# Optimization experiments

Hardware: AMD Instinct MI355X
Metric: run time of the kernel (lower is better)

The kernel has to match this reference:

```python
import jax, jax.numpy as jnp
import numpy as np


def setup_inputs() -> dict:
    key = jax.random.key(0)
    k1, k2, k3 = jax.random.split(key, 3)
    B, M, J = 4096, 64, 24  # batch, n_max_markers, n_joints
    points = jax.random.normal(k1, (B, M, 3), dtype=jnp.float32)
    weight = jax.random.uniform(k2, (B, M, J), dtype=jnp.float32)  # positive soft weights
    offset = jax.random.normal(k3, (B, M, J, 3), dtype=jnp.float32)
    return {"points": points, "weight": weight, "offset": offset}


def reference(points, weight, offset):
    # P: per-joint marker offsets (B, J, 3, M); Q: world marker positions (B, 1, 3, M)
    P = jnp.transpose(offset, (0, 2, 3, 1))
    Q = jnp.transpose(points, (0, 2, 1))[:, None]
    w = jnp.transpose(weight, (0, 2, 1))[:, :, None]  # (B, J, 1, M)

    wsum = jnp.sum(w, axis=-1)                   # (B, J, 1)
    P_ = jnp.sum(P * w, axis=-1) / wsum          # (B, J, 3) weighted centroid of offsets
    Q_ = jnp.sum(Q * w, axis=-1) / wsum          # (B, J, 3) weighted centroid of markers

    X = P - P_[..., None]                        # (B, J, 3, M)
    Y = Q - Q_[..., None]                        # (B, J, 3, M) via broadcast

    # Cross-covariance S = X @ Y^T (NOTE: original multiplies un-weighted centered coords)
    S = jnp.einsum('bjdm,bjem->bjde', X, Y)      # (B, J, 3, 3)

    U, _, Vh = jnp.linalg.svd(S)
    V = jnp.swapaxes(Vh, -1, -2)
    Ut = jnp.swapaxes(U, -1, -2)
    det = jnp.linalg.det(jnp.matmul(V, Ut))      # (B, J) reflection correction
    Ut = Ut.at[..., -1, :].multiply(det[..., None])
    R = jnp.matmul(V, Ut)                        # (B, J, 3, 3) optimal rotation
    t = Q_[..., None] - jnp.matmul(R, P_[..., None])  # (B, J, 3, 1)
    return R, t
```

## Files before the change

### kernel.cpp

```cpp
#include <hip/hip_runtime.h>


constexpr int M = 64;
constexpr int J = 24;
constexpr int NACC = 22;
constexpr int NWS  = 15;

constexpr int L4_W = 0;
constexpr int L4_O = 384;
constexpr int L4_P = 1536;
constexpr int L4_N = 1584;

__global__ __launch_bounds__(256, 4) void accum_kernel(
    const float* __restrict__ points,
    const float* __restrict__ weight,
    const float* __restrict__ offset,
    float* __restrict__ ws,
    int bj_total)
{
    const int b = blockIdx.x;
    const int t = threadIdx.x;

    __shared__ float4 lds4[L4_N];

    const float4* wb4 = (const float4*)(weight + (size_t)b * (M * J));
    const float4* ob4 = (const float4*)(offset + (size_t)b * (M * J * 3));
    const float4* pb4 = (const float4*)(points + (size_t)b * (M * 3));

    float4 o0_ = ob4[t];
    float4 o1_ = ob4[t + 256];
    float4 o2_ = ob4[t + 512];
    float4 o3_ = ob4[t + 768];
    float4 w0_ = wb4[t];
    float4 o4_ = {0.f, 0.f, 0.f, 0.f};
    float4 w1_ = {0.f, 0.f, 0.f, 0.f};
    float4 p0_ = {0.f, 0.f, 0.f, 0.f};
    if (t < 128) { o4_ = ob4[1024 + t]; w1_ = wb4[256 + t]; }
    if (t < 48)  { p0_ = pb4[t]; }

    lds4[L4_O + t]        = o0_;
    lds4[L4_O + 256 + t]  = o1_;
    lds4[L4_O + 512 + t]  = o2_;
    lds4[L4_O + 768 + t]  = o3_;
    lds4[L4_W + t]        = w0_;
    if (t < 128) { lds4[L4_O + 1024 + t] = o4_; lds4[L4_W + 256 + t] = w1_; }
    if (t < 48)  { lds4[L4_P + t] = p0_; }

    __syncthreads();

    const int lane = t & 63;
    const int wv   = t >> 6;
    const int kk   = lane & 7;
    const int jj   = (lane >> 3) + wv * 8;
    if (jj >= J) return;

    const float* w_s = (const float*)lds4;
    const float* o_s = (const float*)lds4 + 4 * L4_O;
    const float* p_s = (const float*)lds4 + 4 * L4_P;

    float acc[NACC];
#pragma unroll
    for (int n = 0; n < NACC; ++n) acc[n] = 0.0f;

#pragma unroll
    for (int i = 0; i < M / 8; ++i) {
        const int m = i * 8 + kk;
        float w  = w_s[m * J + jj];
        float o0 = o_s[m * 72 + jj * 3 + 0];
        float o1 = o_s[m * 72 + jj * 3 + 1];
        float o2 = o_s[m * 72 + jj * 3 + 2];
        float p0 = p_s[m * 3 + 0];
        float p1 = p_s[m * 3 + 1];
        float p2 = p_s[m * 3 + 2];
        acc[0] += w;
        acc[1] = fmaf(w, o0, acc[1]);  acc[2] = fmaf(w, o1, acc[2]);  acc[3] = fmaf(w, o2, acc[3]);
        acc[4] = fmaf(w, p0, acc[4]);  acc[5] = fmaf(w, p1, acc[5]);  acc[6] = fmaf(w, p2, acc[6]);
        acc[7] += o0; acc[8] += o1; acc[9] += o2;
        acc[10] += p0; acc[11] += p1; acc[12] += p2;
        acc[13] = fmaf(o0, p0, acc[13]); acc[14] = fmaf(o0, p1, acc[14]); acc[15] = fmaf(o0, p2, acc[15]);
        acc[16] = fmaf(o1, p0, acc[16]); acc[17] = fmaf(o1, p1, acc[17]); acc[18] = fmaf(o1, p2, acc[18]);
        acc[19] = fmaf(o2, p0, acc[19]); acc[20] = fmaf(o2, p1, acc[20]); acc[21] = fmaf(o2, p2, acc[21]);
    }

#pragma unroll
    for (int n = 0; n < NACC; ++n) {
        float v = acc[n];
        v += __shfl_xor(v, 1);
        v += __shfl_xor(v, 2);
        v += __shfl_xor(v, 4);
        acc[n] = v;
    }

    if (kk != 0) return;

    const float inv = __builtin_amdgcn_rcpf(acc[0]);
    const float cP0 = acc[1] * inv, cP1 = acc[2] * inv, cP2 = acc[3] * inv;
    const float cQ0 = acc[4] * inv, cQ1 = acc[5] * inv, cQ2 = acc[6] * inv;
    const float To0 = acc[7], To1 = acc[8], To2 = acc[9];
    const float Tp0 = acc[10], Tp1 = acc[11], Tp2 = acc[12];
    const float fM = (float)M;
    float Sv[NWS];
    Sv[0] = acc[13] - cP0 * Tp0 - cQ0 * To0 + fM * cP0 * cQ0;
    Sv[1] = acc[14] - cP0 * Tp1 - cQ1 * To0 + fM * cP0 * cQ1;
    Sv[2] = acc[15] - cP0 * Tp2 - cQ2 * To0 + fM * cP0 * cQ2;
    Sv[3] = acc[16] - cP1 * Tp0 - cQ0 * To1 + fM * cP1 * cQ0;
    Sv[4] = acc[17] - cP1 * Tp1 - cQ1 * To1 + fM * cP1 * cQ1;
    Sv[5] = acc[18] - cP1 * Tp2 - cQ2 * To1 + fM * cP1 * cQ2;
    Sv[6] = acc[19] - cP2 * Tp0 - cQ0 * To2 + fM * cP2 * cQ0;
    Sv[7] = acc[20] - cP2 * Tp1 - cQ1 * To2 + fM * cP2 * cQ1;
    Sv[8] = acc[21] - cP2 * Tp2 - cQ2 * To2 + fM * cP2 * cQ2;
    Sv[9]  = cP0; Sv[10] = cP1; Sv[11] = cP2;
    Sv[12] = cQ0; Sv[13] = cQ1; Sv[14] = cQ2;

    const int bj = b * J + jj;
#pragma unroll
    for (int n = 0; n < NWS; ++n) ws[(size_t)n * bj_total + bj] = Sv[n];
}

template<int P, int Q>
__device__ __forceinline__ void jrot(float A[4][4], float V[4][4]) {
    float apq = A[P][Q];
    float theta = (A[Q][Q] - A[P][P]) * __builtin_amdgcn_rcpf(2.0f * apq);
    float t = __builtin_amdgcn_rcpf(fabsf(theta) + __builtin_amdgcn_sqrtf(fmaf(theta, theta, 1.0f)));
    t = (theta < 0.0f) ? -t : t;
    t = (apq == 0.0f) ? 0.0f : t;
    float c = __builtin_amdgcn_rsqf(fmaf(t, t, 1.0f));
    float s = t * c;
#pragma unroll
    for (int k = 0; k < 4; ++k) {
        float akp = A[k][P], akq = A[k][Q];
        A[k][P] = c * akp - s * akq;
        A[k][Q] = s * akp + c * akq;
    }
#pragma unroll
    for (int k = 0; k < 4; ++k) {
        float apk = A[P][k], aqk = A[Q][k];
        A[P][k] = c * apk - s * aqk;
        A[Q][k] = s * apk + c * aqk;
        float vkp = V[k][P], vkq = V[k][Q];
        V[k][P] = c * vkp - s * vkq;
        V[k][Q] = s * vkp + c * vkq;
    }
}

__device__ __forceinline__ void horn_solve(
    float S00, float S01, float S02, float S10, float S11, float S12,
    float S20, float S21, float S22,
    float cP0, float cP1, float cP2, float cQ0, float cQ1, float cQ2,
    float* __restrict__ Rout, float* __restrict__ tout)
{
    float A[4][4], V[4][4];
    A[0][0] = S00 + S11 + S22;
    A[0][1] = A[1][0] = S12 - S21;
    A[0][2] = A[2][0] = S20 - S02;
    A[0][3] = A[3][0] = S01 - S10;
    A[1][1] = S00 - S11 - S22;
    A[1][2] = A[2][1] = S01 + S10;
    A[1][3] = A[3][1] = S02 + S20;
    A[2][2] = -S00 + S11 - S22;
    A[2][3] = A[3][2] = S12 + S21;
    A[3][3] = -S00 - S11 + S22;
#pragma unroll
    for (int r = 0; r < 4; ++r)
#pragma unroll
        for (int c = 0; c < 4; ++c)
            V[r][c] = (r == c) ? 1.0f : 0.0f;

#pragma unroll 1
    for (int sweep = 0; sweep < 6; ++sweep) {
        jrot<0, 1>(A, V); jrot<0, 2>(A, V); jrot<0, 3>(A, V);
        jrot<1, 2>(A, V); jrot<1, 3>(A, V); jrot<2, 3>(A, V);
    }

    float best = A[0][0];
    float qw = V[0][0], qx = V[1][0], qy = V[2][0], qz = V[3][0];
#pragma unroll
    for (int i = 1; i < 4; ++i) {
        bool better = A[i][i] > best;
        best = better ? A[i][i] : best;
        qw = better ? V[0][i] : qw;
        qx = better ? V[1][i] : qx;
        qy = better ? V[2][i] : qy;
        qz = better ? V[3][i] : qz;
    }
    float nrm = __builtin_amdgcn_rsqf(qw * qw + qx * qx + qy * qy + qz * qz);
    qw *= nrm; qx *= nrm; qy *= nrm; qz *= nrm;

    float R00 = 1.f - 2.f * (qy * qy + qz * qz);
    float R01 = 2.f * (qx * qy - qw * qz);
    float R02 = 2.f * (qx * qz + qw * qy);
    float R10 = 2.f * (qx * qy + qw * qz);
    float R11 = 1.f - 2.f * (qx * qx + qz * qz);
    float R12 = 2.f * (qy * qz - qw * qx);
    float R20 = 2.f * (qx * qz - qw * qy);
    float R21 = 2.f * (qy * qz + qw * qx);
    float R22 = 1.f - 2.f * (qx * qx + qy * qy);

    Rout[0] = R00; Rout[1] = R01; Rout[2] = R02;
    Rout[3] = R10; Rout[4] = R11; Rout[5] = R12;
    Rout[6] = R20; Rout[7] = R21; Rout[8] = R22;
    tout[0] = cQ0 - (R00 * cP0 + R01 * cP1 + R02 * cP2);
    tout[1] = cQ1 - (R10 * cP0 + R11 * cP1 + R12 * cP2);
    tout[2] = cQ2 - (R20 * cP0 + R21 * cP1 + R22 * cP2);
}

__global__ __launch_bounds__(64) void solve_kernel(
    const float* __restrict__ ws, float* __restrict__ out, int bj_total)
{
    int tid = blockIdx.x * 64 + threadIdx.x;
    if (tid >= bj_total) return;
    float Sv[NWS];
#pragma unroll
    for (int n = 0; n < NWS; ++n) Sv[n] = ws[(size_t)n * bj_total + tid];
    float Rr[9], tr[3];
    horn_solve(Sv[0], Sv[1], Sv[2], Sv[3], Sv[4], Sv[5], Sv[6], Sv[7], Sv[8],
               Sv[9], Sv[10], Sv[11], Sv[12], Sv[13], Sv[14], Rr, tr);
    float* Rout = out + (size_t)tid * 9;
#pragma unroll
    for (int n = 0; n < 9; ++n) Rout[n] = Rr[n];
    float* tout = out + (size_t)bj_total * 9 + (size_t)tid * 3;
    tout[0] = tr[0]; tout[1] = tr[1]; tout[2] = tr[2];
}

__global__ __launch_bounds__(256) void fused_kernel(
    const float* __restrict__ points, const float* __restrict__ weight,
    const float* __restrict__ offset, float* __restrict__ out, int bj_total)
{
    int tid = blockIdx.x * blockDim.x + threadIdx.x;
    if (tid >= bj_total) return;
    int b = tid / J, j = tid - b * J;
    const float* wq = weight + (size_t)b * M * J + j;
    const float* oq = offset + ((size_t)b * M * J + j) * 3;
    const float* pq = points + (size_t)b * M * 3;
    float a[NACC];
#pragma unroll
    for (int n = 0; n < NACC; ++n) a[n] = 0.0f;
#pragma unroll 4
    for (int m = 0; m < M; ++m) {
        float w = wq[m * J];
        float o0 = oq[m * (J * 3) + 0], o1 = oq[m * (J * 3) + 1], o2 = oq[m * (J * 3) + 2];
        float p0 = pq[m * 3 + 0], p1 = pq[m * 3 + 1], p2 = pq[m * 3 + 2];
        a[0] += w;
        a[1] = fmaf(w, o0, a[1]); a[2] = fmaf(w, o1, a[2]); a[3] = fmaf(w, o2, a[3]);
        a[4] = fmaf(w, p0, a[4]); a[5] = fmaf(w, p1, a[5]); a[6] = fmaf(w, p2, a[6]);
        a[7] += o0; a[8] += o1; a[9] += o2;
        a[10] += p0; a[11] += p1; a[12] += p2;
        a[13] = fmaf(o0, p0, a[13]); a[14] = fmaf(o0, p1, a[14]); a[15] = fmaf(o0, p2, a[15]);
        a[16] = fmaf(o1, p0, a[16]); a[17] = fmaf(o1, p1, a[17]); a[18] = fmaf(o1, p2, a[18]);
        a[19] = fmaf(o2, p0, a[19]); a[20] = fmaf(o2, p1, a[20]); a[21] = fmaf(o2, p2, a[21]);
    }
    float inv = __builtin_amdgcn_rcpf(a[0]);
    float cP0 = a[1] * inv, cP1 = a[2] * inv, cP2 = a[3] * inv;
    float cQ0 = a[4] * inv, cQ1 = a[5] * inv, cQ2 = a[6] * inv;
    const float fM = (float)M;
    float S00 = a[13] - cP0 * a[10] - cQ0 * a[7] + fM * cP0 * cQ0;
    float S01 = a[14] - cP0 * a[11] - cQ1 * a[7] + fM * cP0 * cQ1;
    float S02 = a[15] - cP0 * a[12] - cQ2 * a[7] + fM * cP0 * cQ2;
    float S10 = a[16] - cP1 * a[10] - cQ0 * a[8] + fM * cP1 * cQ0;
    float S11 = a[17] - cP1 * a[11] - cQ1 * a[8] + fM * cP1 * cQ1;
    float S12 = a[18] - cP1 * a[12] - cQ2 * a[8] + fM * cP1 * cQ2;
    float S20 = a[19] - cP2 * a[10] - cQ0 * a[9] + fM * cP2 * cQ0;
    float S21 = a[20] - cP2 * a[11] - cQ1 * a[9] + fM * cP2 * cQ1;
    float S22 = a[21] - cP2 * a[12] - cQ2 * a[9] + fM * cP2 * cQ2;
    float Rr[9], tr[3];
    horn_solve(S00, S01, S02, S10, S11, S12, S20, S21, S22,
               cP0, cP1, cP2, cQ0, cQ1, cQ2, Rr, tr);
    float* Rout = out + (size_t)tid * 9;
#pragma unroll
    for (int n = 0; n < 9; ++n) Rout[n] = Rr[n];
    float* tout = out + (size_t)bj_total * 9 + (size_t)tid * 3;
    tout[0] = tr[0]; tout[1] = tr[1]; tout[2] = tr[2];
}

extern "C" void kernel_launch(void* const* d_in, const int* in_sizes, int n_in,
                              void* d_out, int out_size, void* d_ws, size_t ws_size,
                              hipStream_t stream) {
    const float* points = (const float*)d_in[0];
    const float* weight = (const float*)d_in[1];
    const float* offset = (const float*)d_in[2];
    float* out = (float*)d_out;

    int B = in_sizes[0] / (M * 3);
    int bj_total = B * J;

    size_t need = (size_t)NWS * bj_total * sizeof(float);
    if (ws_size >= need) {
        accum_kernel<<<B, 256, 0, stream>>>(points, weight, offset, (float*)d_ws, bj_total);
        solve_kernel<<<(bj_total + 63) / 64, 64, 0, stream>>>((const float*)d_ws, out, bj_total);
    } else {
        fused_kernel<<<(bj_total + 255) / 256, 256, 0, stream>>>(points, weight, offset, out, bj_total);
    }
}
```

Baseline: 147.7 us.

## Fuse accumulation and Horn solve into one kernel via LDS staging

Merges the accumulation and rotation-solve kernels into a single kernel per batch element. Per-joint covariance and centroid values are written to shared memory instead of a global workspace, then 24 threads per block run the solve and write R and t. This removes a kernel launch and the global workspace write/read. In exchange, the solve runs on a partial wave inside each block after an extra barrier, which may lengthen per-block latency.

```diff
diff --git a/kernel.cpp b/kernel.cpp
--- a/kernel.cpp
+++ b/kernel.cpp
@@ -10,112 +10,6 @@
 constexpr int L4_O = 384;
 constexpr int L4_P = 1536;
 constexpr int L4_N = 1584;
-
-__global__ __launch_bounds__(256, 4) void accum_kernel(
-    const float* __restrict__ points,
-    const float* __restrict__ weight,
-    const float* __restrict__ offset,
-    float* __restrict__ ws,
-    int bj_total)
-{
-    const int b = blockIdx.x;
-    const int t = threadIdx.x;
-
-    __shared__ float4 lds4[L4_N];
-
-    const float4* wb4 = (const float4*)(weight + (size_t)b * (M * J));
-    const float4* ob4 = (const float4*)(offset + (size_t)b * (M * J * 3));
-    const float4* pb4 = (const float4*)(points + (size_t)b * (M * 3));
-
-    float4 o0_ = ob4[t];
-    float4 o1_ = ob4[t + 256];
-    float4 o2_ = ob4[t + 512];
-    float4 o3_ = ob4[t + 768];
-    float4 w0_ = wb4[t];
-    float4 o4_ = {0.f, 0.f, 0.f, 0.f};
-    float4 w1_ = {0.f, 0.f, 0.f, 0.f};
-    float4 p0_ = {0.f, 0.f, 0.f, 0.f};
-    if (t < 128) { o4_ = ob4[1024 + t]; w1_ = wb4[256 + t]; }
-    if (t < 48)  { p0_ = pb4[t]; }
-
-    lds4[L4_O + t]        = o0_;
-    lds4[L4_O + 256 + t]  = o1_;
-    lds4[L4_O + 512 + t]  = o2_;
-    lds4[L4_O + 768 + t]  = o3_;
-    lds4[L4_W + t]        = w0_;
-    if (t < 128) { lds4[L4_O + 1024 + t] = o4_; lds4[L4_W + 256 + t] = w1_; }
-    if (t < 48)  { lds4[L4_P + t] = p0_; }
-
-    __syncthreads();
-
-    const int lane = t & 63;
-    const int wv   = t >> 6;
-    const int kk   = lane & 7;
-    const int jj   = (lane >> 3) + wv * 8;
-    if (jj >= J) return;
-
-    const float* w_s = (const float*)lds4;
-    const float* o_s = (const float*)lds4 + 4 * L4_O;
-    const float* p_s = (const float*)lds4 + 4 * L4_P;
-
-    float acc[NACC];
-#pragma unroll
-    for (int n = 0; n < NACC; ++n) acc[n] = 0.0f;
-
-#pragma unroll
-    for (int i = 0; i < M / 8; ++i) {
-        const int m = i * 8 + kk;
-        float w  = w_s[m * J + jj];
-        float o0 = o_s[m * 72 + jj * 3 + 0];
-        float o1 = o_s[m * 72 + jj * 3 + 1];
-        float o2 = o_s[m * 72 + jj * 3 + 2];
-        float p0 = p_s[m * 3 + 0];
-        float p1 = p_s[m * 3 + 1];
-        float p2 = p_s[m * 3 + 2];
-        acc[0] += w;
-        acc[1] = fmaf(w, o0, acc[1]);  acc[2] = fmaf(w, o1, acc[2]);  acc[3] = fmaf(w, o2, acc[3]);
-        acc[4] = fmaf(w, p0, acc[4]);  acc[5] = fmaf(w, p1, acc[5]);  acc[6] = fmaf(w, p2, acc[6]);
-        acc[7] += o0; acc[8] += o1; acc[9] += o2;
-        acc[10] += p0; acc[11] += p1; acc[12] += p2;
-        acc[13] = fmaf(o0, p0, acc[13]); acc[14] = fmaf(o0, p1, acc[14]); acc[15] = fmaf(o0, p2, acc[15]);
-        acc[16] = fmaf(o1, p0, acc[16]); acc[17] = fmaf(o1, p1, acc[17]); acc[18] = fmaf(o1, p2, acc[18]);
-        acc[19] = fmaf(o2, p0, acc[19]); acc[20] = fmaf(o2, p1, acc[20]); acc[21] = fmaf(o2, p2, acc[21]);
-    }
-
-#pragma unroll
-    for (int n = 0; n < NACC; ++n) {
-        float v = acc[n];
-        v += __shfl_xor(v, 1);
-        v += __shfl_xor(v, 2);
-        v += __shfl_xor(v, 4);
-        acc[n] = v;
-    }
-
-    if (kk != 0) return;
-
-    const float inv = __builtin_amdgcn_rcpf(acc[0]);
-    const float cP0 = acc[1] * inv, cP1 = acc[2] * inv, cP2 = acc[3] * inv;
-    const float cQ0 = acc[4] * inv, cQ1 = acc[5] * inv, cQ2 = acc[6] * inv;
-    const float To0 = acc[7], To1 = acc[8], To2 = acc[9];
-    const float Tp0 = acc[10], Tp1 = acc[11], Tp2 = acc[12];
-    const float fM = (float)M;
-    float Sv[NWS];
-    Sv[0] = acc[13] - cP0 * Tp0 - cQ0 * To0 + fM * cP0 * cQ0;
-    Sv[1] = acc[14] - cP0 * Tp1 - cQ1 * To0 + fM * cP0 * cQ1;
-    Sv[2] = acc[15] - cP0 * Tp2 - cQ2 * To0 + fM * cP0 * cQ2;
-    Sv[3] = acc[16] - cP1 * Tp0 - cQ0 * To1 + fM * cP1 * cQ0;
-    Sv[4] = acc[17] - cP1 * Tp1 - cQ1 * To1 + fM * cP1 * cQ1;
-    Sv[5] = acc[18] - cP1 * Tp2 - cQ2 * To1 + fM * cP1 * cQ2;
-    Sv[6] = acc[19] - cP2 * Tp0 - cQ0 * To2 + fM * cP2 * cQ0;
-    Sv[7] = acc[20] - cP2 * Tp1 - cQ1 * To2 + fM * cP2 * cQ1;
-    Sv[8] = acc[21] - cP2 * Tp2 - cQ2 * To2 + fM * cP2 * cQ2;
-    Sv[9]  = cP0; Sv[10] = cP1; Sv[11] = cP2;
-    Sv[12] = cQ0; Sv[13] = cQ1; Sv[14] = cQ2;
-
-    const int bj = b * J + jj;
-#pragma unroll
-    for (int n = 0; n < NWS; ++n) ws[(size_t)n * bj_total + bj] = Sv[n];
-}
 
 template<int P, int Q>
 __device__ __forceinline__ void jrot(float A[4][4], float V[4][4]) {
@@ -204,72 +98,130 @@
     tout[2] = cQ2 - (R20 * cP0 + R21 * cP1 + R22 * cP2);
 }
 
-__global__ __launch_bounds__(64) void solve_kernel(
-    const float* __restrict__ ws, float* __restrict__ out, int bj_total)
+__global__ __launch_bounds__(256, 4) void kabsch_fused(
+    const float* __restrict__ points,
+    const float* __restrict__ weight,
+    const float* __restrict__ offset,
+    float* __restrict__ out,
+    int bj_total)
 {
-    int tid = blockIdx.x * 64 + threadIdx.x;
-    if (tid >= bj_total) return;
-    float Sv[NWS];
-#pragma unroll
-    for (int n = 0; n < NWS; ++n) Sv[n] = ws[(size_t)n * bj_total + tid];
-    float Rr[9], tr[3];
-    horn_solve(Sv[0], Sv[1], Sv[2], Sv[3], Sv[4], Sv[5], Sv[6], Sv[7], Sv[8],
-               Sv[9], Sv[10], Sv[11], Sv[12], Sv[13], Sv[14], Rr, tr);
-    float* Rout = out + (size_t)tid * 9;
-#pragma unroll
-    for (int n = 0; n < 9; ++n) Rout[n] = Rr[n];
-    float* tout = out + (size_t)bj_total * 9 + (size_t)tid * 3;
-    tout[0] = tr[0]; tout[1] = tr[1]; tout[2] = tr[2];
-}
-
-__global__ __launch_bounds__(256) void fused_kernel(
-    const float* __restrict__ points, const float* __restrict__ weight,
-    const float* __restrict__ offset, float* __restrict__ out, int bj_total)
-{
-    int tid = blockIdx.x * blockDim.x + threadIdx.x;
-    if (tid >= bj_total) return;
-    int b = tid / J, j = tid - b * J;
-    const float* wq = weight + (size_t)b * M * J + j;
-    const float* oq = offset + ((size_t)b * M * J + j) * 3;
-    const float* pq = points + (size_t)b * M * 3;
-    float a[NACC];
-#pragma unroll
-    for (int n = 0; n < NACC; ++n) a[n] = 0.0f;
-#pragma unroll 4
-    for (int m = 0; m < M; ++m) {
-        float w = wq[m * J];
-        float o0 = oq[m * (J * 3) + 0], o1 = oq[m * (J * 3) + 1], o2 = oq[m * (J * 3) + 2];
-        float p0 = pq[m * 3 + 0], p1 = pq[m * 3 + 1], p2 = pq[m * 3 + 2];
-        a[0] += w;
-        a[1] = fmaf(w, o0, a[1]); a[2] = fmaf(w, o1, a[2]); a[3] = fmaf(w, o2, a[3]);
-        a[4] = fmaf(w, p0, a[4]); a[5] = fmaf(w, p1, a[5]); a[6] = fmaf(w, p2, a[6]);
-        a[7] += o0; a[8] += o1; a[9] += o2;
-        a[10] += p0; a[11] += p1; a[12] += p2;
-        a[13] = fmaf(o0, p0, a[13]); a[14] = fmaf(o0, p1, a[14]); a[15] = fmaf(o0, p2, a[15]);
-        a[16] = fmaf(o1, p0, a[16]); a[17] = fmaf(o1, p1, a[17]); a[18] = fmaf(o1, p2, a[18]);
-        a[19] = fmaf(o2, p0, a[19]); a[20] = fmaf(o2, p1, a[20]); a[21] = fmaf(o2, p2, a[21]);
-    }
-    float inv = __builtin_amdgcn_rcpf(a[0]);
-    float cP0 = a[1] * inv, cP1 = a[2] * inv, cP2 = a[3] * inv;
-    float cQ0 = a[4] * inv, cQ1 = a[5] * inv, cQ2 = a[6] * inv;
-    const float fM = (float)M;
-    float S00 = a[13] - cP0 * a[10] - cQ0 * a[7] + fM * cP0 * cQ0;
-    float S01 = a[14] - cP0 * a[11] - cQ1 * a[7] + fM * cP0 * cQ1;
-    float S02 = a[15] - cP0 * a[12] - cQ2 * a[7] + fM * cP0 * cQ2;
-    float S10 = a[16] - cP1 * a[10] - cQ0 * a[8] + fM * cP1 * cQ0;
-    float S11 = a[17] - cP1 * a[11] - cQ1 * a[8] + fM * cP1 * cQ1;
-    float S12 = a[18] - cP1 * a[12] - cQ2 * a[8] + fM * cP1 * cQ2;
-    float S20 = a[19] - cP2 * a[10] - cQ0 * a[9] + fM * cP2 * cQ0;
-    float S21 = a[20] - cP2 * a[11] - cQ1 * a[9] + fM * cP2 * cQ1;
-    float S22 = a[21] - cP2 * a[12] - cQ2 * a[9] + fM * cP2 * cQ2;
-    float Rr[9], tr[3];
-    horn_solve(S00, S01, S02, S10, S11, S12, S20, S21, S22,
-               cP0, cP1, cP2, cQ0, cQ1, cQ2, Rr, tr);
-    float* Rout = out + (size_t)tid * 9;
-#pragma unroll
-    for (int n = 0; n < 9; ++n) Rout[n] = Rr[n];
-    float* tout = out + (size_t)bj_total * 9 + (size_t)tid * 3;
-    tout[0] = tr[0]; tout[1] = tr[1]; tout[2] = tr[2];
+    const int b = blockIdx.x;
+    const int t = threadIdx.x;
+
+    __shared__ float4 lds4[L4_N];
+
+    const float4* wb4 = (const float4*)(weight + (size_t)b * (M * J));
+    const float4* ob4 = (const float4*)(offset + (size_t)b * (M * J * 3));
+    const float4* pb4 = (const float4*)(points + (size_t)b * (M * 3));
+
+    float4 o0_ = ob4[t];
+    float4 o1_ = ob4[t + 256];
+    float4 o2_ = ob4[t + 512];
+    float4 o3_ = ob4[t + 768];
+    float4 w0_ = wb4[t];
+    float4 o4_ = {0.f, 0.f, 0.f, 0.f};
+    float4 w1_ = {0.f, 0.f, 0.f, 0.f};
+    float4 p0_ = {0.f, 0.f, 0.f, 0.f};
+    if (t < 128) { o4_ = ob4[1024 + t]; w1_ = wb4[256 + t]; }
+    if (t < 48)  { p0_ = pb4[t]; }
+
+    lds4[L4_O + t]        = o0_;
+    lds4[L4_O + 256 + t]  = o1_;
+    lds4[L4_O + 512 + t]  = o2_;
+    lds4[L4_O + 768 + t]  = o3_;
+    lds4[L4_W + t]        = w0_;
+    if (t < 128) { lds4[L4_O + 1024 + t] = o4_; lds4[L4_W + 256 + t] = w1_; }
+    if (t < 48)  { lds4[L4_P + t] = p0_; }
+
+    __syncthreads();
+
+    const int lane = t & 63;
+    const int wv   = t >> 6;
+    const int kk   = lane & 7;
+    const int jj   = (lane >> 3) + wv * 8;
+    const bool prod = (jj < J);
+
+    float acc[NACC];
+#pragma unroll
+    for (int n = 0; n < NACC; ++n) acc[n] = 0.0f;
+
+    if (prod) {
+        const float* w_s = (const float*)lds4;
+        const float* o_s = (const float*)lds4 + 4 * L4_O;
+        const float* p_s = (const float*)lds4 + 4 * L4_P;
+
+#pragma unroll
+        for (int i = 0; i < M / 8; ++i) {
+            const int m = i * 8 + kk;
+            float w  = w_s[m * J + jj];
+            float o0 = o_s[m * 72 + jj * 3 + 0];
+            float o1 = o_s[m * 72 + jj * 3 + 1];
+            float o2 = o_s[m * 72 + jj * 3 + 2];
+            float p0 = p_s[m * 3 + 0];
+            float p1 = p_s[m * 3 + 1];
+            float p2 = p_s[m * 3 + 2];
+            acc[0] += w;
+            acc[1] = fmaf(w, o0, acc[1]);  acc[2] = fmaf(w, o1, acc[2]);  acc[3] = fmaf(w, o2, acc[3]);
+            acc[4] = fmaf(w, p0, acc[4]);  acc[5] = fmaf(w, p1, acc[5]);  acc[6] = fmaf(w, p2, acc[6]);
+            acc[7] += o0; acc[8] += o1; acc[9] += o2;
+            acc[10] += p0; acc[11] += p1; acc[12] += p2;
+            acc[13] = fmaf(o0, p0, acc[13]); acc[14] = fmaf(o0, p1, acc[14]); acc[15] = fmaf(o0, p2, acc[15]);
+            acc[16] = fmaf(o1, p0, acc[16]); acc[17] = fmaf(o1, p1, acc[17]); acc[18] = fmaf(o1, p2, acc[18]);
+            acc[19] = fmaf(o2, p0, acc[19]); acc[20] = fmaf(o2, p1, acc[20]); acc[21] = fmaf(o2, p2, acc[21]);
+        }
+
+#pragma unroll
+        for (int n = 0; n < NACC; ++n) {
+            float v = acc[n];
+            v += __shfl_xor(v, 1);
+            v += __shfl_xor(v, 2);
+            v += __shfl_xor(v, 4);
+            acc[n] = v;
+        }
+    }
+
+    __syncthreads();
+
+    float* sv_s = (float*)lds4;
+    if (prod && kk == 0) {
+        const float inv = __builtin_amdgcn_rcpf(acc[0]);
+        const float cP0 = acc[1] * inv, cP1 = acc[2] * inv, cP2 = acc[3] * inv;
+        const float cQ0 = acc[4] * inv, cQ1 = acc[5] * inv, cQ2 = acc[6] * inv;
+        const float To0 = acc[7], To1 = acc[8], To2 = acc[9];
+        const float Tp0 = acc[10], Tp1 = acc[11], Tp2 = acc[12];
+        const float fM = (float)M;
+        float Sv[NWS];
+        Sv[0] = acc[13] - cP0 * Tp0 - cQ0 * To0 + fM * cP0 * cQ0;
+        Sv[1] = acc[14] - cP0 * Tp1 - cQ1 * To0 + fM * cP0 * cQ1;
+        Sv[2] = acc[15] - cP0 * Tp2 - cQ2 * To0 + fM * cP0 * cQ2;
+        Sv[3] = acc[16] - cP1 * Tp0 - cQ0 * To1 + fM * cP1 * cQ0;
+        Sv[4] = acc[17] - cP1 * Tp1 - cQ1 * To1 + fM * cP1 * cQ1;
+        Sv[5] = acc[18] - cP1 * Tp2 - cQ2 * To1 + fM * cP1 * cQ2;
+        Sv[6] = acc[19] - cP2 * Tp0 - cQ0 * To2 + fM * cP2 * cQ0;
+        Sv[7] = acc[20] - cP2 * Tp1 - cQ1 * To2 + fM * cP2 * cQ1;
+        Sv[8] = acc[21] - cP2 * Tp2 - cQ2 * To2 + fM * cP2 * cQ2;
+        Sv[9]  = cP0; Sv[10] = cP1; Sv[11] = cP2;
+        Sv[12] = cQ0; Sv[13] = cQ1; Sv[14] = cQ2;
+#pragma unroll
+        for (int n = 0; n < NWS; ++n) sv_s[n * J + jj] = Sv[n];
+    }
+
+    __syncthreads();
+
+    if (t < J) {
+        float v[NWS];
+#pragma unroll
+        for (int n = 0; n < NWS; ++n) v[n] = sv_s[n * J + t];
+        float Rr[9], tr[3];
+        horn_solve(v[0], v[1], v[2], v[3], v[4], v[5], v[6], v[7], v[8],
+                   v[9], v[10], v[11], v[12], v[13], v[14], Rr, tr);
+        const int bj = b * J + t;
+        float* Rout = out + (size_t)bj * 9;
+#pragma unroll
+        for (int n = 0; n < 9; ++n) Rout[n] = Rr[n];
+        float* tout = out + (size_t)bj_total * 9 + (size_t)bj * 3;
+        tout[0] = tr[0]; tout[1] = tr[1]; tout[2] = tr[2];
+    }
 }
 
 extern "C" void kernel_launch(void* const* d_in, const int* in_sizes, int n_in,
@@ -283,11 +235,5 @@
     int B = in_sizes[0] / (M * 3);
     int bj_total = B * J;
 
-    size_t need = (size_t)NWS * bj_total * sizeof(float);
-    if (ws_size >= need) {
-        accum_kernel<<<B, 256, 0, stream>>>(points, weight, offset, (float*)d_ws, bj_total);
-        solve_kernel<<<(bj_total + 63) / 64, 64, 0, stream>>>((const float*)d_ws, out, bj_total);
-    } else {
-        fused_kernel<<<(bj_total + 255) / 256, 256, 0, stream>>>(points, weight, offset, out, bj_total);
-    }
-}
+    kabsch_fused<<<B, 256, 0, stream>>>(points, weight, offset, out, bj_total);
+}
```

Result: faster. 144.1 us (-2.4%).
